# Kernel tuning notes

Measured on AMD Instinct MI355X. Metric: run time of the kernel, lower is better.

## Reference

```python
import jax, jax.numpy as jnp
import numpy as np

B, H, W, C = 16, 64, 64, 512
HEADS, WS, SHIFT = 16, 8, 4
N = WS * WS            # tokens per window
HID = 4 * C            # mlp hidden


def _buffers():
    # Swin-V2 log-spaced continuous relative coords table [1, 2ws-1, 2ws-1, 2]
    rc = np.arange(-(WS - 1), WS, dtype=np.float32)
    table = np.stack(np.meshgrid(rc, rc, indexing='ij'), axis=-1)[None]
    table = table / (WS - 1) * 8.0
    table = np.sign(table) * np.log2(np.abs(table) + 1.0) / np.log2(8.0)
    # relative position index [N, N]
    coords = np.stack(np.meshgrid(np.arange(WS), np.arange(WS), indexing='ij')).reshape(2, -1)
    rel = (coords[:, :, None] - coords[:, None, :]).transpose(1, 2, 0)
    rel[..., 0] += WS - 1
    rel[..., 1] += WS - 1
    rel[..., 0] *= 2 * WS - 1
    idx = rel.sum(-1).astype(np.int32)
    # shifted-window attention mask [nW, N, N]
    img = np.zeros((H, W), dtype=np.float32)
    sl = (slice(0, -WS), slice(-WS, -SHIFT), slice(-SHIFT, None))
    cnt = 0
    for hs in sl:
        for ws_ in sl:
            img[hs, ws_] = cnt
            cnt += 1
    mw = img.reshape(H // WS, WS, W // WS, WS).transpose(0, 2, 1, 3).reshape(-1, N)
    am = mw[:, None, :] - mw[:, :, None]
    am = np.where(am != 0, np.float32(-100.0), np.float32(0.0)).astype(np.float32)
    return table.astype(np.float32), idx, am


def setup_inputs() -> dict:
    key = jax.random.key(0)
    ks = jax.random.split(key, 8)
    table, idx, am = _buffers()
    p = lambda k, s: jax.random.normal(k, s, jnp.float32) * 0.02
    return {
        'x': jax.random.normal(ks[0], (B, H * W, C), jnp.float32),
        'qkv_w': p(ks[1], (3 * C, C)),
        'q_bias': jnp.zeros((C,), jnp.float32),
        'v_bias': jnp.zeros((C,), jnp.float32),
        'logit_scale': jnp.full((HEADS, 1, 1), np.log(10.0), jnp.float32),
        'cpb_w1': p(ks[2], (512, 2)),
        'cpb_b1': jnp.zeros((512,), jnp.float32),
        'cpb_w2': p(ks[3], (HEADS, 512)),
        'proj_w': p(ks[4], (C, C)),
        'proj_b': jnp.zeros((C,), jnp.float32),
        'norm1_g': jnp.ones((C,), jnp.float32),
        'norm1_b': jnp.zeros((C,), jnp.float32),
        'norm2_g': jnp.ones((C,), jnp.float32),
        'norm2_b': jnp.zeros((C,), jnp.float32),
        'fc1_w': p(ks[5], (HID, C)),
        'fc1_b': jnp.zeros((HID,), jnp.float32),
        'fc2_w': p(ks[6], (C, HID)),
        'fc2_b': jnp.zeros((C,), jnp.float32),
        'coords_table': jnp.asarray(table),
        'attn_mask': jnp.asarray(am),
        'rel_pos_index': jnp.asarray(idx),
    }


def _layernorm(x, g, b):
    m = x.mean(-1, keepdims=True)
    v = ((x - m) ** 2).mean(-1, keepdims=True)
    return (x - m) / jnp.sqrt(v + 1e-5) * g + b


def reference(x, qkv_w, q_bias, v_bias, logit_scale, cpb_w1, cpb_b1, cpb_w2,
              proj_w, proj_b, norm1_g, norm1_b, norm2_g, norm2_b,
              fc1_w, fc1_b, fc2_w, fc2_b, coords_table, attn_mask, rel_pos_index):
    Bsz, L, Cd = x.shape
    d = Cd // HEADS
    shortcut = x
    # cyclic shift + window partition: [B*nW, N, C]
    xr = jnp.roll(x.reshape(Bsz, H, W, Cd), (-SHIFT, -SHIFT), axis=(1, 2))
    xw = xr.reshape(Bsz, H // WS, WS, W // WS, WS, Cd).transpose(0, 1, 3, 2, 4, 5).reshape(-1, N, Cd)
    B_ = xw.shape[0]
    nW = B_ // Bsz
    # qkv with q/v-only bias
    qkv_bias = jnp.concatenate([q_bias, jnp.zeros_like(v_bias), v_bias])
    qkv = (xw @ qkv_w.T + qkv_bias).reshape(B_, N, 3, HEADS, d).transpose(2, 0, 3, 1, 4)
    q, k, v = qkv[0], qkv[1], qkv[2]  # [B_, h, N, d]
    # cosine attention with learned clamped logit scale
    qn = q / jnp.maximum(jnp.linalg.norm(q, axis=-1, keepdims=True), 1e-12)
    kn = k / jnp.maximum(jnp.linalg.norm(k, axis=-1, keepdims=True), 1e-12)
    scale = jnp.exp(jnp.minimum(logit_scale, jnp.log(jnp.float32(100.0))))
    attn = jnp.einsum('bhnd,bhmd->bhnm', qn, kn) * scale
    # CPB MLP relative position bias
    tbl = jax.nn.relu(coords_table @ cpb_w1.T + cpb_b1) @ cpb_w2.T  # [1,2ws-1,2ws-1,h]
    rpb = tbl.reshape(-1, HEADS)[rel_pos_index.reshape(-1)].reshape(N, N, HEADS).transpose(2, 0, 1)
    attn = attn + 16.0 * jax.nn.sigmoid(rpb)[None]
    # shift mask
    attn = (attn.reshape(Bsz, nW, HEADS, N, N) + attn_mask[None, :, None]).reshape(B_, HEADS, N, N)
    attn = jax.nn.softmax(attn, axis=-1)
    out = jnp.einsum('bhnm,bhmd->bhnd', attn, v).transpose(0, 2, 1, 3).reshape(B_, N, Cd)
    out = out @ proj_w.T + proj_b
    # window reverse + reverse shift
    out = out.reshape(Bsz, H // WS, W // WS, WS, WS, Cd).transpose(0, 1, 3, 2, 4, 5).reshape(Bsz, H, W, Cd)
    out = jnp.roll(out, (SHIFT, SHIFT), axis=(1, 2)).reshape(Bsz, L, Cd)
    # Swin-V2 post-norm residuals
    x1 = shortcut + _layernorm(out, norm1_g, norm1_b)
    mlp = jax.nn.gelu(x1 @ fc1_w.T + fc1_b, approximate=False) @ fc2_w.T + fc2_b
    return x1 + _layernorm(mlp, norm2_g, norm2_b)
```

## Files before the change

### kernel.cpp

```cpp
#include <hip/hip_runtime.h>
#include <hip/hip_bf16.h>
#include <math.h>

#define BB     16
#define HH     64
#define WWID   64
#define CCH    512
#define HEADS  16
#define NTOK   64
#define DDIM   32
#define NWIN   64
#define LL     (HH*WWID)
#define MTOT   (BB*LL)
#define BWIN   (BB*NWIN)
#define HIDN   2048
#define SHIFT_ 4

typedef unsigned short u16;
using bf16x8 = __attribute__((ext_vector_type(8))) short;
using f32x4  = __attribute__((ext_vector_type(4))) float;
using f32x16 = __attribute__((ext_vector_type(16))) float;

__device__ __forceinline__ u16 f2bf(float f) {
  union { float f; unsigned u; } v; v.f = f;
  unsigned r = v.u + 0x7fffu + ((v.u >> 16) & 1u);
  return (u16)(r >> 16);
}
__device__ __forceinline__ float bf2f(unsigned h) {
  union { unsigned u; float f; } v; v.u = h << 16;
  return v.f;
}
__device__ __forceinline__ unsigned cvtpk(float lo, float hi) {
  unsigned r;
  asm("v_cvt_pk_bf16_f32 %0, %1, %2" : "=v"(r) : "v"(lo), "v"(hi));
  return r;
}
__device__ __forceinline__ float gelu_f(float v) {
  float v3 = v * v * v;
  float y = 1.5957691216057308f * v + 0.0713548162726009f * v3;
  return v / (1.f + __expf(-y));
}

__device__ __forceinline__ void gload16(const void* g, void* l) {
  __builtin_amdgcn_global_load_lds((const __attribute__((address_space(1))) void*)g,
                                   (__attribute__((address_space(3))) void*)l, 16, 0, 0);
}

__device__ __forceinline__ int win2orig(int b_, int n) {
  int b = b_ >> 6, wi = b_ & 63;
  int hs = (wi >> 3) * 8 + (n >> 3);
  int ws = (wi & 7) * 8 + (n & 7);
  int hq = (hs + SHIFT_) & 63;
  int wq = (ws + SHIFT_) & 63;
  return b * LL + hq * WWID + wq;
}

__global__ void cvt_k(const float* __restrict__ s, u16* __restrict__ d, int n) {
  int i = blockIdx.x * 256 + threadIdx.x;
  if (i < n) d[i] = f2bf(s[i]);
}

__global__ void cpb_k(const float* __restrict__ ct, const float* __restrict__ w1,
                      const float* __restrict__ b1, const float* __restrict__ w2,
                      float* __restrict__ t2) {
  int t = blockIdx.x * 256 + threadIdx.x;
  if (t >= 225 * 16) return;
  int rr = t >> 4, h = t & 15;
  float c0 = ct[rr * 2], c1 = ct[rr * 2 + 1];
  float acc = 0.f;
  for (int j = 0; j < 512; j++) {
    float hv = fmaxf(w1[j * 2] * c0 + w1[j * 2 + 1] * c1 + b1[j], 0.f);
    acc += hv * w2[h * 512 + j];
  }
  t2[t] = acc;
}

__global__ void bias_k(const float* __restrict__ t2, const int* __restrict__ rpi,
                       float* __restrict__ b16) {
  int t = blockIdx.x * 256 + threadIdx.x;
  int nm = t & 4095;
  int h = t >> 12;
  float v = t2[rpi[nm] * 16 + h];
  b16[t] = 16.0f / (1.0f + __expf(-v));
}

__global__ void scale_k(const float* __restrict__ ls, float* __restrict__ sc) {
  int t = threadIdx.x;
  if (t < HEADS) sc[t] = __expf(fminf(ls[t], 4.6051701859880914f));
}

__global__ __launch_bounds__(256) void xw_k(const float* __restrict__ x, u16* __restrict__ xw) {
  int t = blockIdx.x * 256 + threadIdx.x;
  int row = t >> 6;
  int col = (t & 63) * 8;
  const float* src = x + (size_t)win2orig(row >> 6, row & 63) * CCH + col;
  float4 a = *(const float4*)src;
  float4 b = *(const float4*)(src + 4);
  uint4 o = make_uint4(cvtpk(a.x, a.y), cvtpk(a.z, a.w),
                       cvtpk(b.x, b.y), cvtpk(b.z, b.w));
  *(uint4*)(xw + (size_t)row * CCH + col) = o;
}

template<int MODE, int NBN>
__global__ __launch_bounds__(256, 2) void gemm256_k(
    const u16* __restrict__ A, const u16* __restrict__ Bw,
    const float* __restrict__ bias,
    const float* __restrict__ qbias, const float* __restrict__ vbias,
    u16* __restrict__ o0, u16* __restrict__ o1, u16* __restrict__ o2,
    int K, int mchunk)
{
  __shared__ __align__(16) u16 smem[3 * 12288];
  const int t = threadIdx.x;
  const int lin = blockIdx.x;
  const int xcd = lin & 7;
  const int j = lin >> 3;
  const int m0 = (xcd * mchunk + j / NBN) * 256;
  const int n0 = (j % NBN) * 128;
  const int lane = t & 63;
  const int wv = t >> 6;
  const int wm = (wv & 1) * 128;
  const int wn = (wv >> 1) * 64;
  const int l31 = lane & 31;
  const int khalf = lane >> 5;

  const int sstg = (((t >> 2) + (t >> 4)) & 3);
  const int swcol = (((t & 3) ^ sstg) * 8);
  const u16* aP[4]; int aL[4];
  #pragma unroll
  for (int i = 0; i < 4; i++) {
    aP[i] = A + (size_t)(m0 + i * 64 + (t >> 2)) * K + swcol;
    aL[i] = i * 4096 + wv * 1024;
  }
  const u16* bP[2]; int bL[2];
  #pragma unroll
  for (int i = 0; i < 2; i++) {
    bP[i] = Bw + (size_t)(n0 + i * 64 + (t >> 2)) * K + swcol;
    bL[i] = 16384 + i * 4096 + wv * 1024;
  }

  f32x16 acc[4][2] = {};

  auto stage = [&](int k0, int bi) {
    char* base = (char*)smem + bi * 24576;
    #pragma unroll
    for (int i = 0; i < 4; i++) gload16(aP[i] + k0, base + aL[i]);
    #pragma unroll
    for (int i = 0; i < 2; i++) gload16(bP[i] + k0, base + bL[i]);
  };

  const int NT = K >> 5;
  stage(0, 0);
  stage(32, 1);

  const int srd = ((l31 & 3) + ((l31 >> 2) & 3)) & 3;

  for (int it = 0; it < NT; ++it) {
    if (it + 1 < NT) asm volatile("s_waitcnt vmcnt(6)" ::: "memory");
    else             asm volatile("s_waitcnt vmcnt(0)" ::: "memory");
    __builtin_amdgcn_s_barrier();
    asm volatile("" ::: "memory");
    if (it + 2 < NT) stage((it + 2) << 5, (it + 2) % 3);

    const u16* Ab = (const u16*)((const char*)smem + (it % 3) * 24576);
    const u16* Bb = Ab + 8192;
    #pragma unroll
    for (int ks = 0; ks < 2; ks++) {
      const int kc = (ks * 2 + khalf) ^ srd;
      bf16x8 af[4], bf[2];
      #pragma unroll
      for (int mt = 0; mt < 4; mt++)
        af[mt] = *(const bf16x8*)&Ab[(wm + mt * 32 + l31) * 32 + kc * 8];
      #pragma unroll
      for (int nt = 0; nt < 2; nt++)
        bf[nt] = *(const bf16x8*)&Bb[(wn + nt * 32 + l31) * 32 + kc * 8];
      #pragma unroll
      for (int mt = 0; mt < 4; mt++)
        #pragma unroll
        for (int nt = 0; nt < 2; nt++)
          acc[mt][nt] = __builtin_amdgcn_mfma_f32_32x32x16_bf16(bf[nt], af[mt], acc[mt][nt], 0, 0, 0);
    }
  }

  const int part = n0 >> 9;
  u16* qkvdst = (MODE == 0) ? (part == 0 ? o0 : (part == 1 ? o1 : o2)) : o0;
  #pragma unroll
  for (int mt = 0; mt < 4; mt++) {
    const int grow = m0 + wm + mt * 32 + l31;
    size_t rowbase;
    if (MODE == 0) {
      int b_ = grow >> 6, n = grow & 63;
      rowbase = ((size_t)b_ * HEADS) * (NTOK * DDIM) + (size_t)n * DDIM;
    } else if (MODE == 1) {
      rowbase = (size_t)win2orig(grow >> 6, grow & 63) * CCH;
    } else if (MODE == 2) {
      rowbase = (size_t)grow * HIDN;
    } else {
      rowbase = (size_t)grow * CCH;
    }
    #pragma unroll
    for (int nt = 0; nt < 2; nt++) {
      const int cb = n0 + wn + nt * 32;
      unsigned U[4], W[4];
      #pragma unroll
      for (int g = 0; g < 4; g++) {
        const int nb = cb + 8 * g + 4 * khalf;
        float v0 = acc[mt][nt][g * 4 + 0];
        float v1 = acc[mt][nt][g * 4 + 1];
        float v2 = acc[mt][nt][g * 4 + 2];
        float v3 = acc[mt][nt][g * 4 + 3];
        if (MODE == 0) {
          const int cc = nb & 511;
          if (part == 0) {
            float4 b4 = *(const float4*)(qbias + cc);
            v0 += b4.x; v1 += b4.y; v2 += b4.z; v3 += b4.w;
          } else if (part == 2) {
            float4 b4 = *(const float4*)(vbias + cc);
            v0 += b4.x; v1 += b4.y; v2 += b4.z; v3 += b4.w;
          }
        } else {
          float4 b4 = *(const float4*)(bias + nb);
          v0 += b4.x; v1 += b4.y; v2 += b4.z; v3 += b4.w;
          if (MODE == 2) {
            v0 = gelu_f(v0); v1 = gelu_f(v1); v2 = gelu_f(v2); v3 = gelu_f(v3);
          }
        }
        U[g] = cvtpk(v0, v1);
        W[g] = cvtpk(v2, v3);
      }
      asm volatile("v_permlane32_swap_b32 %0, %1" : "+v"(U[0]), "+v"(U[1]));
      asm volatile("v_permlane32_swap_b32 %0, %1" : "+v"(W[0]), "+v"(W[1]));
      asm volatile("v_permlane32_swap_b32 %0, %1" : "+v"(U[2]), "+v"(U[3]));
      asm volatile("v_permlane32_swap_b32 %0, %1" : "+v"(W[2]), "+v"(W[3]));
      uint4 s1 = make_uint4(U[0], W[0], U[1], W[1]);
      uint4 s2 = make_uint4(U[2], W[2], U[3], W[3]);
      if (MODE == 0) {
        const int cc1 = (cb & 511) + 8 * khalf;
        const int cc2 = cc1 + 16;
        *(uint4*)(qkvdst + rowbase + (size_t)(cc1 >> 5) * (NTOK * DDIM) + (cc1 & 31)) = s1;
        *(uint4*)(qkvdst + rowbase + (size_t)(cc2 >> 5) * (NTOK * DDIM) + (cc2 & 31)) = s2;
      } else {
        *(uint4*)(o0 + rowbase + cb + 8 * khalf) = s1;
        *(uint4*)(o0 + rowbase + cb + 16 + 8 * khalf) = s2;
      }
    }
  }
}

__global__ __launch_bounds__(64) void attn_k(
    const u16* __restrict__ qb, const u16* __restrict__ kb, const u16* __restrict__ vb,
    const float* __restrict__ bias16, const float* __restrict__ scale,
    const float* __restrict__ amask, u16* __restrict__ attn_out)
{
  __shared__ u16 Pmat[64][72];
  __shared__ u16 vT[32][72];

  int bh = blockIdx.x;
  int b_ = bh >> 4, h = bh & 15;
  int wi = b_ & 63;
  int lane = threadIdx.x;
  int l15 = lane & 15, quad = lane >> 4;
  const u16* qs = qb + (size_t)bh * (NTOK * DDIM);
  const u16* ks = kb + (size_t)bh * (NTOK * DDIM);
  const u16* vs = vb + (size_t)bh * (NTOK * DDIM);

  bf16x8 qf[4], kf[4];
  #pragma unroll
  for (int mt = 0; mt < 4; mt++) {
    qf[mt] = *(const bf16x8*)(qs + (mt * 16 + l15) * DDIM + quad * 8);
    kf[mt] = *(const bf16x8*)(ks + (mt * 16 + l15) * DDIM + quad * 8);
  }
  #pragma unroll
  for (int mt = 0; mt < 4; mt++) {
    float sq = 0.f, sk = 0.f;
    #pragma unroll
    for (int jj = 0; jj < 8; jj++) {
      float a = bf2f((u16)qf[mt][jj]); sq += a * a;
      float b = bf2f((u16)kf[mt][jj]); sk += b * b;
    }
    sq += __shfl_xor(sq, 16); sq += __shfl_xor(sq, 32);
    sk += __shfl_xor(sk, 16); sk += __shfl_xor(sk, 32);
    float iq = 1.f / fmaxf(sqrtf(sq), 1e-12f);
    float ik = 1.f / fmaxf(sqrtf(sk), 1e-12f);
    #pragma unroll
    for (int jj = 0; jj < 8; jj++) {
      qf[mt][jj] = (short)f2bf(bf2f((u16)qf[mt][jj]) * iq);
      kf[mt][jj] = (short)f2bf(bf2f((u16)kf[mt][jj]) * ik);
    }
  }
  f32x4 s[4][4];
  #pragma unroll
  for (int mt = 0; mt < 4; mt++)
    #pragma unroll
    for (int nt = 0; nt < 4; nt++) {
      f32x4 c = {0.f, 0.f, 0.f, 0.f};
      s[mt][nt] = __builtin_amdgcn_mfma_f32_16x16x32_bf16(qf[mt], kf[nt], c, 0, 0, 0);
    }
  #pragma unroll
  for (int d8 = 0; d8 < 4; d8++) {
    bf16x8 vv = *(const bf16x8*)(vs + lane * DDIM + d8 * 8);
    #pragma unroll
    for (int jj = 0; jj < 8; jj++) vT[d8 * 8 + jj][lane] = (u16)vv[jj];
  }

  float sc = scale[h];
  float rinv[4][4];
  const float* bbase = bias16 + (size_t)h * 4096;
  const float* mbase = amask + (size_t)wi * 4096;
  #pragma unroll
  for (int mt = 0; mt < 4; mt++) {
    #pragma unroll
    for (int i = 0; i < 4; i++) {
      int row = mt * 16 + quad * 4 + i;
      const float* bro = bbase + row * 64;
      const float* mro = mbase + row * 64;
      float p[4];
      float mx = -1e30f;
      #pragma unroll
      for (int nt = 0; nt < 4; nt++) {
        int col = nt * 16 + l15;
        float vv = s[mt][nt][i] * sc + bro[col] + mro[col];
        p[nt] = vv;
        mx = fmaxf(mx, vv);
      }
      mx = fmaxf(mx, __shfl_xor(mx, 1));
      mx = fmaxf(mx, __shfl_xor(mx, 2));
      mx = fmaxf(mx, __shfl_xor(mx, 4));
      mx = fmaxf(mx, __shfl_xor(mx, 8));
      float sum = 0.f;
      #pragma unroll
      for (int nt = 0; nt < 4; nt++) {
        float e = __expf(p[nt] - mx);
        p[nt] = e;
        sum += e;
      }
      sum += __shfl_xor(sum, 1);
      sum += __shfl_xor(sum, 2);
      sum += __shfl_xor(sum, 4);
      sum += __shfl_xor(sum, 8);
      rinv[mt][i] = 1.f / sum;
      #pragma unroll
      for (int nt = 0; nt < 4; nt++)
        Pmat[row][nt * 16 + l15] = f2bf(p[nt]);
    }
  }
  __syncthreads();

  f32x4 oacc[4][2] = {};
  #pragma unroll
  for (int ks2 = 0; ks2 < 2; ks2++) {
    bf16x8 pf[4], vf[2];
    #pragma unroll
    for (int mt = 0; mt < 4; mt++)
      pf[mt] = *(const bf16x8*)&Pmat[mt * 16 + l15][ks2 * 32 + quad * 8];
    #pragma unroll
    for (int nt = 0; nt < 2; nt++)
      vf[nt] = *(const bf16x8*)&vT[nt * 16 + l15][ks2 * 32 + quad * 8];
    #pragma unroll
    for (int mt = 0; mt < 4; mt++)
      #pragma unroll
      for (int nt = 0; nt < 2; nt++)
        oacc[mt][nt] = __builtin_amdgcn_mfma_f32_16x16x32_bf16(pf[mt], vf[nt], oacc[mt][nt], 0, 0, 0);
  }
  #pragma unroll
  for (int mt = 0; mt < 4; mt++)
    #pragma unroll
    for (int nt = 0; nt < 2; nt++)
      #pragma unroll
      for (int i = 0; i < 4; i++) {
        int n = mt * 16 + quad * 4 + i;
        int d = nt * 16 + l15;
        float val = oacc[mt][nt][i] * rinv[mt][i];
        attn_out[(size_t)(b_ * 64 + n) * CCH + h * DDIM + d] = f2bf(val);
      }
}

__global__ __launch_bounds__(256) void ln_res_k(
    const float* __restrict__ xin, const u16* __restrict__ pin,
    const float* __restrict__ gam, const float* __restrict__ bet,
    float* __restrict__ x1f, u16* __restrict__ x1b)
{
  int row = blockIdx.x * 4 + (threadIdx.x >> 6);
  int lane = threadIdx.x & 63;
  size_t base = (size_t)row * CCH + lane * 8;
  uint4 u = *(const uint4*)(pin + base);
  unsigned w[4] = {u.x, u.y, u.z, u.w};
  float pv[8];
  #pragma unroll
  for (int j = 0; j < 4; j++) {
    pv[j * 2] = bf2f(w[j] & 0xffffu);
    pv[j * 2 + 1] = bf2f(w[j] >> 16);
  }
  float4 x0 = *(const float4*)(xin + base);
  float4 x1 = *(const float4*)(xin + base + 4);
  float xr[8] = {x0.x, x0.y, x0.z, x0.w, x1.x, x1.y, x1.z, x1.w};
  float s = 0.f, sq = 0.f;
  #pragma unroll
  for (int j = 0; j < 8; j++) { s += pv[j]; sq += pv[j] * pv[j]; }
  #pragma unroll
  for (int o = 32; o > 0; o >>= 1) { s += __shfl_xor(s, o, 64); sq += __shfl_xor(sq, o, 64); }
  float mean = s * (1.0f / 512.0f);
  float var = sq * (1.0f / 512.0f) - mean * mean;
  float rstd = rsqrtf(var + 1e-5f);
  float4 g0 = *(const float4*)(gam + lane * 8);
  float4 g1 = *(const float4*)(gam + lane * 8 + 4);
  float4 b0 = *(const float4*)(bet + lane * 8);
  float4 b1 = *(const float4*)(bet + lane * 8 + 4);
  float gg[8] = {g0.x, g0.y, g0.z, g0.w, g1.x, g1.y, g1.z, g1.w};
  float bb[8] = {b0.x, b0.y, b0.z, b0.w, b1.x, b1.y, b1.z, b1.w};
  float val[8];
  #pragma unroll
  for (int j = 0; j < 8; j++)
    val[j] = xr[j] + (pv[j] - mean) * rstd * gg[j] + bb[j];
  *(float4*)(x1f + base)     = make_float4(val[0], val[1], val[2], val[3]);
  *(float4*)(x1f + base + 4) = make_float4(val[4], val[5], val[6], val[7]);
  *(uint4*)(x1b + base) = make_uint4(cvtpk(val[0], val[1]), cvtpk(val[2], val[3]),
                                     cvtpk(val[4], val[5]), cvtpk(val[6], val[7]));
}

__global__ __launch_bounds__(256) void ln_fin_k(
    const u16* __restrict__ mlp, const float* __restrict__ gam,
    const float* __restrict__ bet, float* __restrict__ io)
{
  int row = blockIdx.x * 4 + (threadIdx.x >> 6);
  int lane = threadIdx.x & 63;
  size_t base = (size_t)row * CCH + lane * 8;
  uint4 u = *(const uint4*)(mlp + base);
  unsigned w[4] = {u.x, u.y, u.z, u.w};
  float pv[8];
  #pragma unroll
  for (int j = 0; j < 4; j++) {
    pv[j * 2] = bf2f(w[j] & 0xffffu);
    pv[j * 2 + 1] = bf2f(w[j] >> 16);
  }
  float s = 0.f, sq = 0.f;
  #pragma unroll
  for (int j = 0; j < 8; j++) { s += pv[j]; sq += pv[j] * pv[j]; }
  #pragma unroll
  for (int o = 32; o > 0; o >>= 1) { s += __shfl_xor(s, o, 64); sq += __shfl_xor(sq, o, 64); }
  float mean = s * (1.0f / 512.0f);
  float var = sq * (1.0f / 512.0f) - mean * mean;
  float rstd = rsqrtf(var + 1e-5f);
  float4 g0 = *(const float4*)(gam + lane * 8);
  float4 g1 = *(const float4*)(gam + lane * 8 + 4);
  float4 b0 = *(const float4*)(bet + lane * 8);
  float4 b1 = *(const float4*)(bet + lane * 8 + 4);
  float gg[8] = {g0.x, g0.y, g0.z, g0.w, g1.x, g1.y, g1.z, g1.w};
  float bb[8] = {b0.x, b0.y, b0.z, b0.w, b1.x, b1.y, b1.z, b1.w};
  float4 i0 = *(const float4*)(io + base);
  float4 i1 = *(const float4*)(io + base + 4);
  float iv[8] = {i0.x, i0.y, i0.z, i0.w, i1.x, i1.y, i1.z, i1.w};
  float out[8];
  #pragma unroll
  for (int j = 0; j < 8; j++)
    out[j] = iv[j] + (pv[j] - mean) * rstd * gg[j] + bb[j];
  *(float4*)(io + base)     = make_float4(out[0], out[1], out[2], out[3]);
  *(float4*)(io + base + 4) = make_float4(out[4], out[5], out[6], out[7]);
}

#define OFF_Q     ((size_t)0)
#define OFF_K     ((size_t)67108864)
#define OFF_V     ((size_t)134217728)
#define OFF_ATTN  ((size_t)201326592)
#define OFF_X1B   ((size_t)268435456)
#define OFF_WQKV  ((size_t)335544320)
#define OFF_WPROJ ((size_t)337117184)
#define OFF_WFC1  ((size_t)337641472)
#define OFF_WFC2  ((size_t)339738624)
#define OFF_T2    ((size_t)341835776)
#define OFF_B16   ((size_t)341852160)
#define OFF_SC    ((size_t)342114304)

extern "C" void kernel_launch(void* const* d_in, const int* in_sizes, int n_in,
                              void* d_out, int out_size, void* d_ws, size_t ws_size,
                              hipStream_t stream) {
  const float* x        = (const float*)d_in[0];
  const float* qkv_w    = (const float*)d_in[1];
  const float* q_bias   = (const float*)d_in[2];
  const float* v_bias   = (const float*)d_in[3];
  const float* lscale   = (const float*)d_in[4];
  const float* cpb_w1   = (const float*)d_in[5];
  const float* cpb_b1   = (const float*)d_in[6];
  const float* cpb_w2   = (const float*)d_in[7];
  const float* proj_w   = (const float*)d_in[8];
  const float* proj_b   = (const float*)d_in[9];
  const float* n1g      = (const float*)d_in[10];
  const float* n1b      = (const float*)d_in[11];
  const float* n2g      = (const float*)d_in[12];
  const float* n2b      = (const float*)d_in[13];
  const float* fc1_w    = (const float*)d_in[14];
  const float* fc1_b    = (const float*)d_in[15];
  const float* fc2_w    = (const float*)d_in[16];
  const float* fc2_b    = (const float*)d_in[17];
  const float* ctab     = (const float*)d_in[18];
  const float* amask    = (const float*)d_in[19];
  const int*   rpi      = (const int*)d_in[20];

  char* ws = (char*)d_ws;
  float* outp = (float*)d_out;

  u16*   q_buf    = (u16*)(ws + OFF_Q);
  u16*   k_buf    = (u16*)(ws + OFF_K);
  u16*   v_buf    = (u16*)(ws + OFF_V);
  u16*   proj_out = (u16*)(ws + OFF_Q);
  u16*   hid      = (u16*)(ws + OFF_Q);
  u16*   xw       = (u16*)(ws + OFF_ATTN);
  u16*   attn_out = (u16*)(ws + OFF_ATTN);
  u16*   mlp_out  = (u16*)(ws + OFF_ATTN);
  u16*   x1b      = (u16*)(ws + OFF_X1B);
  u16*   wqkv     = (u16*)(ws + OFF_WQKV);
  u16*   wproj    = (u16*)(ws + OFF_WPROJ);
  u16*   wfc1     = (u16*)(ws + OFF_WFC1);
  u16*   wfc2     = (u16*)(ws + OFF_WFC2);
  float* t2       = (float*)(ws + OFF_T2);
  float* b16      = (float*)(ws + OFF_B16);
  float* scbuf    = (float*)(ws + OFF_SC);

  cvt_k<<<(1536 * 512 + 255) / 256, 256, 0, stream>>>(qkv_w, wqkv, 1536 * 512);
  cvt_k<<<(512 * 512 + 255) / 256, 256, 0, stream>>>(proj_w, wproj, 512 * 512);
  cvt_k<<<(2048 * 512 + 255) / 256, 256, 0, stream>>>(fc1_w, wfc1, 2048 * 512);
  cvt_k<<<(512 * 2048 + 255) / 256, 256, 0, stream>>>(fc2_w, wfc2, 512 * 2048);
  cpb_k<<<15, 256, 0, stream>>>(ctab, cpb_w1, cpb_b1, cpb_w2, t2);
  bias_k<<<256, 256, 0, stream>>>(t2, rpi, b16);
  scale_k<<<1, 64, 0, stream>>>(lscale, scbuf);

  xw_k<<<MTOT * 64 / 256, 256, 0, stream>>>(x, xw);
  gemm256_k<0, 12><<<256 * 12, 256, 0, stream>>>(
      xw, wqkv, nullptr, q_bias, v_bias, q_buf, k_buf, v_buf, 512, 32);
  attn_k<<<BWIN * HEADS, 64, 0, stream>>>(q_buf, k_buf, v_buf, b16, scbuf, amask, attn_out);
  gemm256_k<1, 4><<<256 * 4, 256, 0, stream>>>(
      attn_out, wproj, proj_b, nullptr, nullptr, proj_out, nullptr, nullptr, 512, 32);
  ln_res_k<<<MTOT / 4, 256, 0, stream>>>(x, proj_out, n1g, n1b, outp, x1b);
  for (int half = 0; half < 2; half++) {
    const u16* a1 = x1b + (size_t)half * (MTOT / 2) * CCH;
    u16* m1 = mlp_out + (size_t)half * (MTOT / 2) * CCH;
    gemm256_k<2, 16><<<128 * 16, 256, 0, stream>>>(
        a1, wfc1, fc1_b, nullptr, nullptr, hid, nullptr, nullptr, 512, 16);
    gemm256_k<3, 4><<<128 * 4, 256, 0, stream>>>(
        hid, wfc2, fc2_b, nullptr, nullptr, m1, nullptr, nullptr, 2048, 16);
  }
  ln_fin_k<<<MTOT / 4, 256, 0, stream>>>(mlp_out, n2g, n2b, outp);
}
```

Baseline: 1.052 ms.

## Load GEMM weight fragments directly into double-buffered registers instead of LDS

Stops staging the B (weight) tile through shared memory. Each wave now loads its B MFMA fragments straight from global memory into registers, double-buffered across an unrolled-by-two K loop, while A keeps the 3-stage LDS pipeline. This shrinks LDS use per block and removes the B LDS writes and reads plus their bank traffic. In exchange, the per-lane B global loads are less coalesced, are duplicated across the two M-waves, and add register pressure; the vmcnt bookkeeping also changes.

```diff
diff --git a/kernel.cpp b/kernel.cpp
--- a/kernel.cpp
+++ b/kernel.cpp
@@ -109,7 +109,7 @@
     u16* __restrict__ o0, u16* __restrict__ o1, u16* __restrict__ o2,
     int K, int mchunk)
 {
-  __shared__ __align__(16) u16 smem[3 * 12288];
+  __shared__ __align__(16) u16 smem[3 * 8192];
   const int t = threadIdx.x;
   const int lin = blockIdx.x;
   const int xcd = lin & 7;
@@ -131,54 +131,66 @@
     aP[i] = A + (size_t)(m0 + i * 64 + (t >> 2)) * K + swcol;
     aL[i] = i * 4096 + wv * 1024;
   }
-  const u16* bP[2]; int bL[2];
-  #pragma unroll
-  for (int i = 0; i < 2; i++) {
-    bP[i] = Bw + (size_t)(n0 + i * 64 + (t >> 2)) * K + swcol;
-    bL[i] = 16384 + i * 4096 + wv * 1024;
-  }
+  const u16* bReg[2];
+  #pragma unroll
+  for (int nt = 0; nt < 2; nt++)
+    bReg[nt] = Bw + (size_t)(n0 + wn + nt * 32 + l31) * K + khalf * 8;
 
   f32x16 acc[4][2] = {};
 
   auto stage = [&](int k0, int bi) {
-    char* base = (char*)smem + bi * 24576;
+    char* base = (char*)smem + bi * 16384;
     #pragma unroll
     for (int i = 0; i < 4; i++) gload16(aP[i] + k0, base + aL[i]);
-    #pragma unroll
-    for (int i = 0; i < 2; i++) gload16(bP[i] + k0, base + bL[i]);
   };
 
   const int NT = K >> 5;
   stage(0, 0);
   stage(32, 1);
+  bf16x8 bfA[2][2], bfB[2][2];
+  #pragma unroll
+  for (int nt = 0; nt < 2; nt++)
+    #pragma unroll
+    for (int ks = 0; ks < 2; ks++)
+      bfA[nt][ks] = *(const bf16x8*)(bReg[nt] + ks * 16);
 
   const int srd = ((l31 & 3) + ((l31 >> 2) & 3)) & 3;
 
-  for (int it = 0; it < NT; ++it) {
-    if (it + 1 < NT) asm volatile("s_waitcnt vmcnt(6)" ::: "memory");
-    else             asm volatile("s_waitcnt vmcnt(0)" ::: "memory");
+  auto body = [&](int it, bf16x8 (&cur)[2][2], bf16x8 (&nxt)[2][2]) {
+    if (it + 1 < NT) asm volatile("s_waitcnt vmcnt(8)" ::: "memory");
+    else             asm volatile("s_waitcnt vmcnt(4)" ::: "memory");
     __builtin_amdgcn_s_barrier();
     asm volatile("" ::: "memory");
+
+    if (it + 1 < NT) {
+      const int kn = (it + 1) << 5;
+      #pragma unroll
+      for (int nt = 0; nt < 2; nt++)
+        #pragma unroll
+        for (int ks = 0; ks < 2; ks++)
+          nxt[nt][ks] = *(const bf16x8*)(bReg[nt] + kn + ks * 16);
+    }
     if (it + 2 < NT) stage((it + 2) << 5, (it + 2) % 3);
 
-    const u16* Ab = (const u16*)((const char*)smem + (it % 3) * 24576);
-    const u16* Bb = Ab + 8192;
+    const u16* Ab = (const u16*)((const char*)smem + (it % 3) * 16384);
     #pragma unroll
     for (int ks = 0; ks < 2; ks++) {
       const int kc = (ks * 2 + khalf) ^ srd;
-      bf16x8 af[4], bf[2];
+      bf16x8 af[4];
       #pragma unroll
       for (int mt = 0; mt < 4; mt++)
         af[mt] = *(const bf16x8*)&Ab[(wm + mt * 32 + l31) * 32 + kc * 8];
-      #pragma unroll
-      for (int nt = 0; nt < 2; nt++)
-        bf[nt] = *(const bf16x8*)&Bb[(wn + nt * 32 + l31) * 32 + kc * 8];
       #pragma unroll
       for (int mt = 0; mt < 4; mt++)
         #pragma unroll
         for (int nt = 0; nt < 2; nt++)
-          acc[mt][nt] = __builtin_amdgcn_mfma_f32_32x32x16_bf16(bf[nt], af[mt], acc[mt][nt], 0, 0, 0);
-    }
+          acc[mt][nt] = __builtin_amdgcn_mfma_f32_32x32x16_bf16(cur[nt][ks], af[mt], acc[mt][nt], 0, 0, 0);
+    }
+  };
+
+  for (int it2 = 0; it2 < NT; it2 += 2) {
+    body(it2, bfA, bfB);
+    body(it2 + 1, bfB, bfA);
   }
 
   const int part = n0 >> 9;
```

After: 1.221 ms. 16.0% more time.

## Rewrite GEMM as 256x256 tile, 8-wave, 16x16 MFMA with phased double buffering

Applied to the files above, without the earlier changes.

The GEMM kernel moves from a 256x128 tile with 4 waves and 32x32x16 MFMA to a 256x256 tile with 8 waves, 64-wide K steps and 16x16x32 MFMA. Loading is restructured into four phases per K step: the next tile's global-to-LDS loads are interleaved between MFMA clusters, with barriers, s_setprio and sched_barrier used to overlap memory with compute. The larger tile raises data reuse per block and halves grid sizes, at the cost of 128KB of LDS, more accumulator registers, more barriers, and narrower uint2 epilogue stores.

```diff
diff --git a/kernel.cpp b/kernel.cpp
--- a/kernel.cpp
+++ b/kernel.cpp
@@ -19,7 +19,6 @@
 typedef unsigned short u16;
 using bf16x8 = __attribute__((ext_vector_type(8))) short;
 using f32x4  = __attribute__((ext_vector_type(4))) float;
-using f32x16 = __attribute__((ext_vector_type(16))) float;
 
 __device__ __forceinline__ u16 f2bf(float f) {
   union { float f; unsigned u; } v; v.f = f;
@@ -102,90 +101,141 @@
 }
 
 template<int MODE, int NBN>
-__global__ __launch_bounds__(256, 2) void gemm256_k(
+__global__ __launch_bounds__(512, 2) void gemm256_k(
     const u16* __restrict__ A, const u16* __restrict__ Bw,
     const float* __restrict__ bias,
     const float* __restrict__ qbias, const float* __restrict__ vbias,
     u16* __restrict__ o0, u16* __restrict__ o1, u16* __restrict__ o2,
     int K, int mchunk)
 {
-  __shared__ __align__(16) u16 smem[3 * 12288];
+  __shared__ __align__(16) u16 smem[2 * 32768];
   const int t = threadIdx.x;
   const int lin = blockIdx.x;
   const int xcd = lin & 7;
   const int j = lin >> 3;
   const int m0 = (xcd * mchunk + j / NBN) * 256;
-  const int n0 = (j % NBN) * 128;
+  const int n0 = (j % NBN) * 256;
   const int lane = t & 63;
   const int wv = t >> 6;
-  const int wm = (wv & 1) * 128;
-  const int wn = (wv >> 1) * 64;
-  const int l31 = lane & 31;
-  const int khalf = lane >> 5;
-
-  const int sstg = (((t >> 2) + (t >> 4)) & 3);
-  const int swcol = (((t & 3) ^ sstg) * 8);
-  const u16* aP[4]; int aL[4];
-  #pragma unroll
-  for (int i = 0; i < 4; i++) {
-    aP[i] = A + (size_t)(m0 + i * 64 + (t >> 2)) * K + swcol;
-    aL[i] = i * 4096 + wv * 1024;
-  }
-  const u16* bP[2]; int bL[2];
-  #pragma unroll
-  for (int i = 0; i < 2; i++) {
-    bP[i] = Bw + (size_t)(n0 + i * 64 + (t >> 2)) * K + swcol;
-    bL[i] = 16384 + i * 4096 + wv * 1024;
-  }
-
-  f32x16 acc[4][2] = {};
-
-  auto stage = [&](int k0, int bi) {
-    char* base = (char*)smem + bi * 24576;
-    #pragma unroll
-    for (int i = 0; i < 4; i++) gload16(aP[i] + k0, base + aL[i]);
-    #pragma unroll
-    for (int i = 0; i < 2; i++) gload16(bP[i] + k0, base + bL[i]);
+  const int wr = wv >> 2;
+  const int wc = wv & 3;
+  const int l15 = lane & 15;
+  const int l4 = lane >> 4;
+
+  const int rl = t >> 3;
+  const int cg = (t & 7) ^ ((t >> 3) & 7);
+  const int ck0 = (l4) ^ (lane & 7);
+  const int ck1 = (4 + l4) ^ (lane & 7);
+
+  auto stageU = [&](int T, int u, int bi) {
+    const u16* mat = (u < 2) ? A : Bw;
+    const int gbase = ((u < 2) ? m0 : n0) + (u & 1) * 128;
+    size_t roff = (size_t)(gbase + rl) * K + (size_t)T * 64 + cg * 8;
+    char* lds = (char*)smem + bi * 65536 + (u >= 2 ? 32768 : 0) + (u & 1) * 16384 + wv * 1024;
+    gload16(mat + roff, lds);
+    gload16(mat + roff + (size_t)64 * K, lds + 8192);
   };
 
-  const int NT = K >> 5;
-  stage(0, 0);
-  stage(32, 1);
-
-  const int srd = ((l31 & 3) + ((l31 >> 2) & 3)) & 3;
+  f32x4 acc[8][4] = {};
+
+  const int NT = K >> 6;
+  #pragma unroll
+  for (int u = 0; u < 4; u++) stageU(0, u, 0);
+  asm volatile("s_waitcnt vmcnt(0)" ::: "memory");
+  __builtin_amdgcn_s_barrier();
 
   for (int it = 0; it < NT; ++it) {
-    if (it + 1 < NT) asm volatile("s_waitcnt vmcnt(6)" ::: "memory");
-    else             asm volatile("s_waitcnt vmcnt(0)" ::: "memory");
-    __builtin_amdgcn_s_barrier();
-    asm volatile("" ::: "memory");
-    if (it + 2 < NT) stage((it + 2) << 5, (it + 2) % 3);
-
-    const u16* Ab = (const u16*)((const char*)smem + (it % 3) * 24576);
-    const u16* Bb = Ab + 8192;
-    #pragma unroll
-    for (int ks = 0; ks < 2; ks++) {
-      const int kc = (ks * 2 + khalf) ^ srd;
-      bf16x8 af[4], bf[2];
-      #pragma unroll
-      for (int mt = 0; mt < 4; mt++)
-        af[mt] = *(const bf16x8*)&Ab[(wm + mt * 32 + l31) * 32 + kc * 8];
-      #pragma unroll
-      for (int nt = 0; nt < 2; nt++)
-        bf[nt] = *(const bf16x8*)&Bb[(wn + nt * 32 + l31) * 32 + kc * 8];
-      #pragma unroll
-      for (int mt = 0; mt < 4; mt++)
+    const int cur = it & 1, nxt = cur ^ 1;
+    const u16* bufA = smem + cur * 32768;
+    const u16* bufB = bufA + 16384;
+    const bool st = (it + 1 < NT);
+    bf16x8 bfr[4];
+
+    {
+      bf16x8 afr[4];
+      #pragma unroll
+      for (int nf = 0; nf < 4; nf++)
+        bfr[nf] = *(const bf16x8*)&bufB[(wc * 64 + nf * 16 + l15) * 64 + ck0 * 8];
+      #pragma unroll
+      for (int fm = 0; fm < 4; fm++)
+        afr[fm] = *(const bf16x8*)&bufA[(wr * 128 + fm * 16 + l15) * 64 + ck0 * 8];
+      if (st) { stageU(it + 1, 0, nxt); stageU(it + 1, 1, nxt); }
+      __builtin_amdgcn_s_barrier();
+      asm volatile("s_waitcnt lgkmcnt(0)" ::: "memory");
+      __builtin_amdgcn_sched_barrier(0);
+      __builtin_amdgcn_s_setprio(1);
+      #pragma unroll
+      for (int fm = 0; fm < 4; fm++)
         #pragma unroll
-        for (int nt = 0; nt < 2; nt++)
-          acc[mt][nt] = __builtin_amdgcn_mfma_f32_32x32x16_bf16(bf[nt], af[mt], acc[mt][nt], 0, 0, 0);
+        for (int nf = 0; nf < 4; nf++)
+          acc[fm][nf] = __builtin_amdgcn_mfma_f32_16x16x32_bf16(bfr[nf], afr[fm], acc[fm][nf], 0, 0, 0);
+      __builtin_amdgcn_s_setprio(0);
+      __builtin_amdgcn_s_barrier();
+    }
+    {
+      bf16x8 afr[4];
+      #pragma unroll
+      for (int fm = 0; fm < 4; fm++)
+        afr[fm] = *(const bf16x8*)&bufA[(wr * 128 + 64 + fm * 16 + l15) * 64 + ck0 * 8];
+      if (st) { stageU(it + 1, 2, nxt); stageU(it + 1, 3, nxt); }
+      __builtin_amdgcn_s_barrier();
+      asm volatile("s_waitcnt lgkmcnt(0)" ::: "memory");
+      __builtin_amdgcn_sched_barrier(0);
+      __builtin_amdgcn_s_setprio(1);
+      #pragma unroll
+      for (int fm = 0; fm < 4; fm++)
+        #pragma unroll
+        for (int nf = 0; nf < 4; nf++)
+          acc[4 + fm][nf] = __builtin_amdgcn_mfma_f32_16x16x32_bf16(bfr[nf], afr[fm], acc[4 + fm][nf], 0, 0, 0);
+      __builtin_amdgcn_s_setprio(0);
+      __builtin_amdgcn_s_barrier();
+    }
+    {
+      bf16x8 afr[4];
+      #pragma unroll
+      for (int nf = 0; nf < 4; nf++)
+        bfr[nf] = *(const bf16x8*)&bufB[(wc * 64 + nf * 16 + l15) * 64 + ck1 * 8];
+      #pragma unroll
+      for (int fm = 0; fm < 4; fm++)
+        afr[fm] = *(const bf16x8*)&bufA[(wr * 128 + fm * 16 + l15) * 64 + ck1 * 8];
+      __builtin_amdgcn_s_barrier();
+      asm volatile("s_waitcnt lgkmcnt(0)" ::: "memory");
+      __builtin_amdgcn_sched_barrier(0);
+      __builtin_amdgcn_s_setprio(1);
+      #pragma unroll
+      for (int fm = 0; fm < 4; fm++)
+        #pragma unroll
+        for (int nf = 0; nf < 4; nf++)
+          acc[fm][nf] = __builtin_amdgcn_mfma_f32_16x16x32_bf16(bfr[nf], afr[fm], acc[fm][nf], 0, 0, 0);
+      __builtin_amdgcn_s_setprio(0);
+      __builtin_amdgcn_s_barrier();
+    }
+    {
+      bf16x8 afr[4];
+      #pragma unroll
+      for (int fm = 0; fm < 4; fm++)
+        afr[fm] = *(const bf16x8*)&bufA[(wr * 128 + 64 + fm * 16 + l15) * 64 + ck1 * 8];
+      __builtin_amdgcn_s_barrier();
+      asm volatile("s_waitcnt lgkmcnt(0)" ::: "memory");
+      __builtin_amdgcn_sched_barrier(0);
+      __builtin_amdgcn_s_setprio(1);
+      #pragma unroll
+      for (int fm = 0; fm < 4; fm++)
+        #pragma unroll
+        for (int nf = 0; nf < 4; nf++)
+          acc[4 + fm][nf] = __builtin_amdgcn_mfma_f32_16x16x32_bf16(bfr[nf], afr[fm], acc[4 + fm][nf], 0, 0, 0);
+      __builtin_amdgcn_s_setprio(0);
+      asm volatile("s_waitcnt vmcnt(0)" ::: "memory");
+      __builtin_amdgcn_s_barrier();
     }
   }
 
   const int part = n0 >> 9;
   u16* qkvdst = (MODE == 0) ? (part == 0 ? o0 : (part == 1 ? o1 : o2)) : o0;
-  #pragma unroll
-  for (int mt = 0; mt < 4; mt++) {
-    const int grow = m0 + wm + mt * 32 + l31;
+  const int l4q = l4 * 4;
+  #pragma unroll
+  for (int mf = 0; mf < 8; mf++) {
+    const int grow = m0 + wr * 128 + mf * 16 + l15;
     size_t rowbase;
     if (MODE == 0) {
       int b_ = grow >> 6, n = grow & 63;
@@ -198,49 +248,35 @@
       rowbase = (size_t)grow * CCH;
     }
     #pragma unroll
-    for (int nt = 0; nt < 2; nt++) {
-      const int cb = n0 + wn + nt * 32;
-      unsigned U[4], W[4];
-      #pragma unroll
-      for (int g = 0; g < 4; g++) {
-        const int nb = cb + 8 * g + 4 * khalf;
-        float v0 = acc[mt][nt][g * 4 + 0];
-        float v1 = acc[mt][nt][g * 4 + 1];
-        float v2 = acc[mt][nt][g * 4 + 2];
-        float v3 = acc[mt][nt][g * 4 + 3];
-        if (MODE == 0) {
-          const int cc = nb & 511;
-          if (part == 0) {
-            float4 b4 = *(const float4*)(qbias + cc);
-            v0 += b4.x; v1 += b4.y; v2 += b4.z; v3 += b4.w;
-          } else if (part == 2) {
-            float4 b4 = *(const float4*)(vbias + cc);
-            v0 += b4.x; v1 += b4.y; v2 += b4.z; v3 += b4.w;
-          }
-        } else {
-          float4 b4 = *(const float4*)(bias + nb);
+    for (int nf = 0; nf < 4; nf++) {
+      const int n = n0 + wc * 64 + nf * 16 + l4q;
+      float v0 = acc[mf][nf][0];
+      float v1 = acc[mf][nf][1];
+      float v2 = acc[mf][nf][2];
+      float v3 = acc[mf][nf][3];
+      if (MODE == 0) {
+        const int cc = n & 511;
+        if (part == 0) {
+          float4 b4 = *(const float4*)(qbias + cc);
           v0 += b4.x; v1 += b4.y; v2 += b4.z; v3 += b4.w;
-          if (MODE == 2) {
-            v0 = gelu_f(v0); v1 = gelu_f(v1); v2 = gelu_f(v2); v3 = gelu_f(v3);
-          }
+        } else if (part == 2) {
+          float4 b4 = *(const float4*)(vbias + cc);
+          v0 += b4.x; v1 += b4.y; v2 += b4.z; v3 += b4.w;
         }
-        U[g] = cvtpk(v0, v1);
-        W[g] = cvtpk(v2, v3);
+      } else {
+        float4 b4 = *(const float4*)(bias + n);
+        v0 += b4.x; v1 += b4.y; v2 += b4.z; v3 += b4.w;
+        if (MODE == 2) {
+          v0 = gelu_f(v0); v1 = gelu_f(v1); v2 = gelu_f(v2); v3 = gelu_f(v3);
+        }
       }
-      asm volatile("v_permlane32_swap_b32 %0, %1" : "+v"(U[0]), "+v"(U[1]));
-      asm volatile("v_permlane32_swap_b32 %0, %1" : "+v"(W[0]), "+v"(W[1]));
-      asm volatile("v_permlane32_swap_b32 %0, %1" : "+v"(U[2]), "+v"(U[3]));
-      asm volatile("v_permlane32_swap_b32 %0, %1" : "+v"(W[2]), "+v"(W[3]));
-      uint4 s1 = make_uint4(U[0], W[0], U[1], W[1]);
-      uint4 s2 = make_uint4(U[2], W[2], U[3], W[3]);
+      uint2 pk = make_uint2(cvtpk(v0, v1), cvtpk(v2, v3));
       if (MODE == 0) {
-        const int cc1 = (cb & 511) + 8 * khalf;
-        const int cc2 = cc1 + 16;
-        *(uint4*)(qkvdst + rowbase + (size_t)(cc1 >> 5) * (NTOK * DDIM) + (cc1 & 31)) = s1;
-        *(uint4*)(qkvdst + rowbase + (size_t)(cc2 >> 5) * (NTOK * DDIM) + (cc2 & 31)) = s2;
+        const int cc = n & 511;
+        const int hh = cc >> 5, dd = cc & 31;
+        *(uint2*)(qkvdst + rowbase + (size_t)hh * (NTOK * DDIM) + dd) = pk;
       } else {
-        *(uint4*)(o0 + rowbase + cb + 8 * khalf) = s1;
-        *(uint4*)(o0 + rowbase + cb + 16 + 8 * khalf) = s2;
+        *(uint2*)(o0 + rowbase + n) = pk;
       }
     }
   }
@@ -524,18 +560,18 @@
   scale_k<<<1, 64, 0, stream>>>(lscale, scbuf);
 
   xw_k<<<MTOT * 64 / 256, 256, 0, stream>>>(x, xw);
-  gemm256_k<0, 12><<<256 * 12, 256, 0, stream>>>(
+  gemm256_k<0, 6><<<256 * 6, 512, 0, stream>>>(
       xw, wqkv, nullptr, q_bias, v_bias, q_buf, k_buf, v_buf, 512, 32);
   attn_k<<<BWIN * HEADS, 64, 0, stream>>>(q_buf, k_buf, v_buf, b16, scbuf, amask, attn_out);
-  gemm256_k<1, 4><<<256 * 4, 256, 0, stream>>>(
+  gemm256_k<1, 2><<<256 * 2, 512, 0, stream>>>(
       attn_out, wproj, proj_b, nullptr, nullptr, proj_out, nullptr, nullptr, 512, 32);
   ln_res_k<<<MTOT / 4, 256, 0, stream>>>(x, proj_out, n1g, n1b, outp, x1b);
   for (int half = 0; half < 2; half++) {
     const u16* a1 = x1b + (size_t)half * (MTOT / 2) * CCH;
     u16* m1 = mlp_out + (size_t)half * (MTOT / 2) * CCH;
-    gemm256_k<2, 16><<<128 * 16, 256, 0, stream>>>(
+    gemm256_k<2, 8><<<128 * 8, 512, 0, stream>>>(
         a1, wfc1, fc1_b, nullptr, nullptr, hid, nullptr, nullptr, 512, 16);
-    gemm256_k<3, 4><<<128 * 4, 256, 0, stream>>>(
+    gemm256_k<3, 2><<<128 * 2, 512, 0, stream>>>(
         hid, wfc2, fc2_b, nullptr, nullptr, m1, nullptr, nullptr, 2048, 16);
   }
   ln_fin_k<<<MTOT / 4, 256, 0, stream>>>(mlp_out, n2g, n2b, outp);
```

Result: no change. 1.041 ms (-1.1%).
